# Performance work log

Hardware: AMD Instinct MI355X
Metric: run time of the kernel (lower is better)

The kernel has to match this reference:

```python
import jax, jax.numpy as jnp
import numpy as np

N_NODES = 50000
N_REL = 3
N_EDGES = 640000
D_IN = 128
D_HID = 128
D_OUT = 32
N_LAYERS = 2


def setup_inputs() -> dict:
    key = jax.random.key(0)
    ks = jax.random.split(key, 7)
    x = jax.random.normal(ks[0], (N_NODES, D_IN), dtype=jnp.float32)
    edge_index = jax.random.randint(ks[1], (N_REL, 2, N_EDGES), 0, N_NODES, dtype=jnp.int32)
    sc = 1.0 / np.sqrt(D_HID)
    W_neigh = jax.random.normal(ks[2], (N_LAYERS, N_REL, D_IN, D_HID), dtype=jnp.float32) * sc
    W_root = jax.random.normal(ks[3], (N_LAYERS, N_REL, D_IN, D_HID), dtype=jnp.float32) * sc
    b_conv = jax.random.normal(ks[4], (N_LAYERS, N_REL, D_HID), dtype=jnp.float32) * sc
    lin_W = jax.random.normal(ks[5], (D_HID, D_OUT), dtype=jnp.float32) * sc
    lin_b = jax.random.normal(ks[6], (D_OUT,), dtype=jnp.float32) * sc
    return {"x": x, "edge_index": edge_index, "W_neigh": W_neigh,
            "W_root": W_root, "b_conv": b_conv, "lin_W": lin_W, "lin_b": lin_b}


def _sage_hetero_layer(h, edge_index, Wn_l, Wr_l, b_l):
    # h: [N, d_in]; edge_index: [n_rel, 2, E]
    N = h.shape[0]
    acc = jnp.zeros((N, Wn_l.shape[-1]), dtype=h.dtype)
    for r in range(edge_index.shape[0]):  # small fixed relation set
        src, dst = edge_index[r, 0], edge_index[r, 1]
        msg = h[src]                                         # gather [E, d]
        summed = jax.ops.segment_sum(msg, dst, num_segments=N)
        deg = jax.ops.segment_sum(jnp.ones(src.shape, h.dtype), dst, num_segments=N)
        mean = summed / jnp.maximum(deg, 1.0)[:, None]       # SAGE mean aggr
        # SAGEConv: lin_l(aggr) + lin_r(x); bias lives in lin_l
        acc = acc + mean @ Wn_l[r] + h @ Wr_l[r] + b_l[r]    # HeteroConv sum across relations
    return acc


def reference(x, edge_index, W_neigh, W_root, b_conv, lin_W, lin_b):
    h = x
    for l in range(W_neigh.shape[0]):
        h = jax.nn.relu(_sage_hetero_layer(h, edge_index, W_neigh[l], W_root[l], b_conv[l]))
    return h @ lin_W + lin_b
```

## Files before the change

### kernel.cpp

```cpp
#include <hip/hip_runtime.h>

#define NN 50000
#define NE 640000
#define NR 3
#define DH 128
#define ET (NR * NE)

#define BK 256
#define NBK 196
#define NBT (NR * NBK)
#define NCH 512
#define CH (ET / NCH)
#define CAPB 4096

typedef __attribute__((ext_vector_type(8))) short short8;
typedef __attribute__((ext_vector_type(4))) float f32x4;
typedef __attribute__((ext_vector_type(2))) float f32x2;

__device__ __forceinline__ float bf2f(uint u) { return __uint_as_float(u << 16); }
__device__ __forceinline__ uint f2bf(float f) {
    uint u = __float_as_uint(f);
    u += 0x7fff + ((u >> 16) & 1);
    return u >> 16;
}
__device__ __forceinline__ uint pack2(float a, float b) { return f2bf(a) | (f2bf(b) << 16); }
__device__ __forceinline__ uint pk2t(float a, float b) {
    return __builtin_amdgcn_perm(__float_as_uint(b), __float_as_uint(a), 0x07060302u);
}
__device__ __forceinline__ f32x2 pkadd(f32x2 a, f32x2 b) {
    f32x2 d;
    asm("v_pk_add_f32 %0, %1, %2" : "=v"(d) : "v"(a), "v"(b));
    return d;
}
__device__ __forceinline__ f32x2 f8lo(uint u) {
    return __builtin_amdgcn_cvt_pk_f32_fp8(u, false);
}
__device__ __forceinline__ f32x2 f8hi(uint u) {
    return __builtin_amdgcn_cvt_pk_f32_fp8(u, true);
}
__device__ __forceinline__ uint pack4f8(float a, float b, float c, float d) {
    int w = __builtin_amdgcn_cvt_pk_fp8_f32(a, b, 0, false);
    w = __builtin_amdgcn_cvt_pk_fp8_f32(c, d, w, true);
    return (uint)w;
}

__global__ __launch_bounds__(256) void prep_hist(const float* __restrict__ x,
                                                 const int* __restrict__ ei,
                                                 const float* __restrict__ Wn,
                                                 const float* __restrict__ Wr,
                                                 const float* __restrict__ bc,
                                                 const float* __restrict__ linW,
                                                 unsigned char* __restrict__ xf8,
                                                 ushort* __restrict__ Wpack,
                                                 float* __restrict__ bsum,
                                                 int* __restrict__ gcnt) {
    int bid = blockIdx.x;
    int t = threadIdx.x;
    if (bid < NCH) {
        __shared__ int hist[NBT];
        for (int i = t; i < NBT; i += 256) hist[i] = 0;
        __syncthreads();
        int e0 = bid * CH;
        for (int i = t; i < CH; i += 256) {
            int e = e0 + i;
            int r = (e >= 2 * NE) ? 2 : (e >= NE ? 1 : 0);
            int le = e - r * NE;
            int dst = ei[r * 2 * NE + NE + le];
            atomicAdd(&hist[r * NBK + (dst >> 8)], 1);
        }
        __syncthreads();
        for (int i = t; i < NBT; i += 256) gcnt[bid * NBT + i] = hist[i];
    } else if (bid < NCH + 6251) {
        int gid = (bid - NCH) * 256 + t;
        if (gid >= NN * DH / 4) return;
        float4 v = ((const float4*)x)[gid];
        ((uint*)xf8)[gid] = pack4f8(v.x, v.y, v.z, v.w);
    } else if (bid < NCH + 6251 + 66) {
        int tid = (bid - NCH - 6251) * 256 + t;
        if (tid >= 264 * 64) return;
        int f = tid >> 6, lane = tid & 63;
        int l15 = lane & 15, l4 = lane >> 4;
        ushort hi8[8], lo8[8];
        if (f < 256) {
            int layer = f >> 7, seg = (f >> 5) & 3, kc = (f >> 3) & 3, nb = f & 7;
            int col = nb * 16 + l15;
            int kb = kc * 32 + l4 * 8;
#pragma unroll
            for (int e = 0; e < 8; ++e) {
                int k = kb + e;
                float v;
                if (seg < 3) {
                    v = Wn[(((size_t)layer * 3 + seg) * 128 + k) * 128 + col];
                } else {
                    const float* base = Wr + (size_t)layer * 3 * 16384;
                    v = base[k * 128 + col] + base[16384 + k * 128 + col] +
                        base[32768 + k * 128 + col];
                }
                uint h = f2bf(v);
                float rem = v - bf2f(h);
                hi8[e] = (ushort)h;
                lo8[e] = (ushort)f2bf(rem);
            }
        } else {
            int g = f - 256;
            int kc = g >> 1, nb = g & 1;
            int col = nb * 16 + l15;
            int kb = kc * 32 + l4 * 8;
#pragma unroll
            for (int e = 0; e < 8; ++e) {
                float v = linW[(kb + e) * 32 + col];
                uint h = f2bf(v);
                float rem = v - bf2f(h);
                hi8[e] = (ushort)h;
                lo8[e] = (ushort)f2bf(rem);
            }
        }
        *(short8*)(Wpack + (size_t)f * 1024 + lane * 8) = *(short8*)hi8;
        *(short8*)(Wpack + (size_t)f * 1024 + 512 + lane * 8) = *(short8*)lo8;
    } else {
        int l = t >> 7, j = t & 127;
        const float* bb = bc + l * 3 * DH;
        bsum[t] = bb[j] + bb[DH + j] + bb[2 * DH + j];
    }
}

__global__ __launch_bounds__(256) void cscan_kernel(const int* __restrict__ gcnt,
                                                    int* __restrict__ gbase,
                                                    int* __restrict__ btot) {
    int b = blockIdx.x, t = threadIdx.x;
    int v0 = gcnt[(2 * t) * NBT + b];
    int v1 = gcnt[(2 * t + 1) * NBT + b];
    int s = v0 + v1;
    int lane = t & 63, w = t >> 6;
    int sc = s;
#pragma unroll
    for (int d = 1; d < 64; d <<= 1) {
        int u = __shfl_up(sc, d);
        if (lane >= d) sc += u;
    }
    __shared__ int ws[4];
    if (lane == 63) ws[w] = sc;
    __syncthreads();
    int add = 0;
#pragma unroll
    for (int q = 0; q < 3; ++q)
        if (q < w) add += ws[q];
    int incl = sc + add;
    int excl = incl - s;
    gbase[(2 * t) * NBT + b] = excl;
    gbase[(2 * t + 1) * NBT + b] = excl + v0;
    if (t == 255) btot[b] = incl;
}

__global__ __launch_bounds__(256) void scatter_kernel(const int* __restrict__ ei,
                                                      const int* __restrict__ gbase,
                                                      uint* __restrict__ pairs) {
    __shared__ int cur[NBT];
    int g = blockIdx.x, t = threadIdx.x;
    for (int i = t; i < NBT; i += 256) cur[i] = i * CAPB + gbase[g * NBT + i];
    __syncthreads();
    int e0 = g * CH;
    for (int i = t; i < CH; i += 256) {
        int e = e0 + i;
        int r = (e >= 2 * NE) ? 2 : (e >= NE ? 1 : 0);
        int le = e - r * NE;
        int src = ei[r * 2 * NE + le];
        int dst = ei[r * 2 * NE + NE + le];
        int b = r * NBK + (dst >> 8);
        int pos = atomicAdd(&cur[b], 1);
        pairs[pos] = ((uint)src << 8) | (uint)(dst & 255u);
    }
}

__global__ __launch_bounds__(256) void csr_kernel(const uint* __restrict__ pairs,
                                                  const int* __restrict__ btot,
                                                  int* __restrict__ csr,
                                                  int2* __restrict__ od) {
    int b = blockIdx.x;
    int r = b / NBK;
    int n0 = (b - r * NBK) * BK;
    int cnt = btot[b];
    int base = b * CAPB;
    int t = threadIdx.x;

    __shared__ int hist[BK];
    __shared__ int cur[BK];
    __shared__ int ws[4];
    hist[t] = 0;
    __syncthreads();
    const uint* pp = pairs + base;
    for (int i = t; i < cnt; i += 256) atomicAdd(&hist[pp[i] & 255u], 1);
    __syncthreads();

    int lane = t & 63, w = t >> 6;
    int v = hist[t], s = v;
#pragma unroll
    for (int d = 1; d < 64; d <<= 1) {
        int u = __shfl_up(s, d);
        if (lane >= d) s += u;
    }
    if (lane == 63) ws[w] = s;
    __syncthreads();
    int add = 0;
#pragma unroll
    for (int q = 0; q < 3; ++q)
        if (q < w) add += ws[q];
    int excl = s + add - v;

    int node = n0 + t;
    if (node < NN) od[r * NN + node] = make_int2(base + excl, v);
    cur[t] = excl;
    __syncthreads();

    for (int i = t; i < cnt; i += 256) {
        uint pk = pp[i];
        int pos = atomicAdd(&cur[pk & 255u], 1);
        csr[base + pos] = (int)(pk >> 8);
    }
}

__global__ __launch_bounds__(256) void aggr_kernel(const unsigned char* __restrict__ tb8,
                                                   unsigned char* __restrict__ mean8,
                                                   const int* __restrict__ csr,
                                                   const int2* __restrict__ od) {
    int gtask = (blockIdx.x * 256 + threadIdx.x) >> 3;
    if (gtask >= NR * NN) return;
    int cs = threadIdx.x & 7;
    int2 v2 = od[gtask];
    int base = v2.x, d = v2.y;
    const int* lst = csr + base;
    const unsigned char* tbc = tb8 + cs * 16;

    f32x2 a2[8] = {{0.f, 0.f}, {0.f, 0.f}, {0.f, 0.f}, {0.f, 0.f},
                   {0.f, 0.f}, {0.f, 0.f}, {0.f, 0.f}, {0.f, 0.f}};
    for (int e = 0; e < d; e += 8) {
        uint4 q[8];
#pragma unroll
        for (int k = 0; k < 8; ++k) {
            int ee = e + k;
            int idx = lst[min(ee, d - 1)];
            uint4 v = *(const uint4*)(tbc + (size_t)idx * DH);
            bool ok = ee < d;
            q[k].x = ok ? v.x : 0u;
            q[k].y = ok ? v.y : 0u;
            q[k].z = ok ? v.z : 0u;
            q[k].w = ok ? v.w : 0u;
        }
#pragma unroll
        for (int k = 0; k < 8; ++k) {
            a2[0] = pkadd(a2[0], f8lo(q[k].x));
            a2[1] = pkadd(a2[1], f8hi(q[k].x));
            a2[2] = pkadd(a2[2], f8lo(q[k].y));
            a2[3] = pkadd(a2[3], f8hi(q[k].y));
            a2[4] = pkadd(a2[4], f8lo(q[k].z));
            a2[5] = pkadd(a2[5], f8hi(q[k].z));
            a2[6] = pkadd(a2[6], f8lo(q[k].w));
            a2[7] = pkadd(a2[7], f8hi(q[k].w));
        }
    }
    float inv = 1.f / fmaxf((float)d, 1.f);
    uint4 o;
    o.x = pack4f8(a2[0].x * inv, a2[0].y * inv, a2[1].x * inv, a2[1].y * inv);
    o.y = pack4f8(a2[2].x * inv, a2[2].y * inv, a2[3].x * inv, a2[3].y * inv);
    o.z = pack4f8(a2[4].x * inv, a2[4].y * inv, a2[5].x * inv, a2[5].y * inv);
    o.w = pack4f8(a2[6].x * inv, a2[6].y * inv, a2[7].x * inv, a2[7].y * inv);
    *(uint4*)(mean8 + (size_t)gtask * DH + cs * 16) = o;
}

template <bool LAST>
__global__ __launch_bounds__(256) void gemm_mfma(
    const float* __restrict__ xroot,
    const ushort* __restrict__ tbroot,
    const unsigned char* __restrict__ mean8,
    void* __restrict__ h_out,
    unsigned char* __restrict__ h1f8,
    const ushort* __restrict__ Wp,
    const float* __restrict__ bsum,
    const ushort* __restrict__ lWp,
    const float* __restrict__ linb)
{
    __shared__ ushort As[64][136];

    const int t = threadIdx.x, lane = t & 63, w = t >> 6;
    const int l15 = lane & 15, l4 = lane >> 4;
    const int row0 = blockIdx.x * 64;

    f32x4 acc[4][2];
    {
        float4 b0 = *(const float4*)(bsum + (2 * w) * 16 + l4 * 4);
        float4 b1 = *(const float4*)(bsum + (2 * w + 1) * 16 + l4 * 4);
#pragma unroll
        for (int rt = 0; rt < 4; ++rt) {
            acc[rt][0] = f32x4{b0.x, b0.y, b0.z, b0.w};
            acc[rt][1] = f32x4{b1.x, b1.y, b1.z, b1.w};
        }
    }

    for (int seg = 0; seg < 4; ++seg) {
        __syncthreads();
        if (seg < NR) {
#pragma unroll
            for (int i = 0; i < 2; ++i) {
                int q = i * 256 + t;
                int r = q >> 3, c = q & 7;
                int node = row0 + r;
                uint4 o0 = make_uint4(0, 0, 0, 0), o1 = make_uint4(0, 0, 0, 0);
                if (node < NN) {
                    uint4 v = *(const uint4*)(mean8 + ((size_t)seg * NN + node) * DH + c * 16);
                    f32x2 lo, hi;
                    lo = f8lo(v.x); hi = f8hi(v.x);
                    o0.x = pk2t(lo.x, lo.y); o0.y = pk2t(hi.x, hi.y);
                    lo = f8lo(v.y); hi = f8hi(v.y);
                    o0.z = pk2t(lo.x, lo.y); o0.w = pk2t(hi.x, hi.y);
                    lo = f8lo(v.z); hi = f8hi(v.z);
                    o1.x = pk2t(lo.x, lo.y); o1.y = pk2t(hi.x, hi.y);
                    lo = f8lo(v.w); hi = f8hi(v.w);
                    o1.z = pk2t(lo.x, lo.y); o1.w = pk2t(hi.x, hi.y);
                }
                *(uint4*)(&As[r][c * 16]) = o0;
                *(uint4*)(&As[r][c * 16 + 8]) = o1;
            }
        } else {
#pragma unroll
            for (int i = 0; i < 4; ++i) {
                int q = i * 256 + t;
                int r = q >> 4, c = q & 15;
                int node = row0 + r;
                uint4 v = make_uint4(0, 0, 0, 0);
                if (node < NN) {
                    if constexpr (!LAST) {
                        float4 f0 = *(const float4*)(xroot + (size_t)node * DH + c * 8);
                        float4 f1 = *(const float4*)(xroot + (size_t)node * DH + c * 8 + 4);
                        v.x = pack2(f0.x, f0.y);
                        v.y = pack2(f0.z, f0.w);
                        v.z = pack2(f1.x, f1.y);
                        v.w = pack2(f1.z, f1.w);
                    } else {
                        v = *(const uint4*)(tbroot + (size_t)node * DH + c * 8);
                    }
                }
                *(uint4*)(&As[r][c * 8]) = v;
            }
        }
        __syncthreads();
        const ushort* wseg = Wp + (size_t)seg * 32768;
#pragma unroll
        for (int kc = 0; kc < 4; ++kc) {
            const ushort* wkc = wseg + kc * 8192;
            short8 bh0 = *(const short8*)(wkc + (2 * w) * 1024 + lane * 8);
            short8 bl0 = *(const short8*)(wkc + (2 * w) * 1024 + 512 + lane * 8);
            short8 bh1 = *(const short8*)(wkc + (2 * w + 1) * 1024 + lane * 8);
            short8 bl1 = *(const short8*)(wkc + (2 * w + 1) * 1024 + 512 + lane * 8);
#pragma unroll
            for (int rt = 0; rt < 4; ++rt) {
                short8 a = *(const short8*)(&As[rt * 16 + l15][kc * 32 + l4 * 8]);
                acc[rt][0] = __builtin_amdgcn_mfma_f32_16x16x32_bf16(bh0, a, acc[rt][0], 0, 0, 0);
                acc[rt][0] = __builtin_amdgcn_mfma_f32_16x16x32_bf16(bl0, a, acc[rt][0], 0, 0, 0);
                acc[rt][1] = __builtin_amdgcn_mfma_f32_16x16x32_bf16(bh1, a, acc[rt][1], 0, 0, 0);
                acc[rt][1] = __builtin_amdgcn_mfma_f32_16x16x32_bf16(bl1, a, acc[rt][1], 0, 0, 0);
            }
        }
    }

    if constexpr (!LAST) {
        ushort* hb = (ushort*)h_out;
#pragma unroll
        for (int rt = 0; rt < 4; ++rt) {
            int node = row0 + rt * 16 + l15;
            if (node < NN) {
#pragma unroll
                for (int j = 0; j < 2; ++j) {
                    int c0 = (2 * w + j) * 16 + l4 * 4;
                    float r0 = fmaxf(acc[rt][j][0], 0.f);
                    float r1 = fmaxf(acc[rt][j][1], 0.f);
                    float r2 = fmaxf(acc[rt][j][2], 0.f);
                    float r3 = fmaxf(acc[rt][j][3], 0.f);
                    uint2 o;
                    o.x = pack2(r0, r1);
                    o.y = pack2(r2, r3);
                    *(uint2*)(hb + (size_t)node * DH + c0) = o;
                    *(uint*)(h1f8 + (size_t)node * DH + c0) = pack4f8(r0, r1, r2, r3);
                }
            }
        }
    } else {
        __syncthreads();
#pragma unroll
        for (int rt = 0; rt < 4; ++rt) {
            int rl = rt * 16 + l15;
#pragma unroll
            for (int j = 0; j < 2; ++j) {
                int c0 = (2 * w + j) * 16 + l4 * 4;
                uint2 o;
                o.x = pack2(fmaxf(acc[rt][j][0], 0.f), fmaxf(acc[rt][j][1], 0.f));
                o.y = pack2(fmaxf(acc[rt][j][2], 0.f), fmaxf(acc[rt][j][3], 0.f));
                *(uint2*)(&As[rl][c0]) = o;
            }
        }
        __syncthreads();
        f32x4 acc2[2];
        {
            float4 c0 = *(const float4*)(linb + l4 * 4);
            float4 c1 = *(const float4*)(linb + 16 + l4 * 4);
            acc2[0] = f32x4{c0.x, c0.y, c0.z, c0.w};
            acc2[1] = f32x4{c1.x, c1.y, c1.z, c1.w};
        }
#pragma unroll
        for (int kc = 0; kc < 4; ++kc) {
            short8 a = *(const short8*)(&As[w * 16 + l15][kc * 32 + l4 * 8]);
#pragma unroll
            for (int j = 0; j < 2; ++j) {
                short8 bh = *(const short8*)(lWp + (kc * 2 + j) * 1024 + lane * 8);
                short8 bl = *(const short8*)(lWp + (kc * 2 + j) * 1024 + 512 + lane * 8);
                acc2[j] = __builtin_amdgcn_mfma_f32_16x16x32_bf16(bh, a, acc2[j], 0, 0, 0);
                acc2[j] = __builtin_amdgcn_mfma_f32_16x16x32_bf16(bl, a, acc2[j], 0, 0, 0);
            }
        }
        float* outp = (float*)h_out;
        int node = row0 + w * 16 + l15;
        if (node < NN) {
#pragma unroll
            for (int j = 0; j < 2; ++j) {
                *(f32x4*)(outp + (size_t)node * 32 + j * 16 + l4 * 4) = acc2[j];
            }
        }
    }
}

extern "C" void kernel_launch(void* const* d_in, const int* in_sizes, int n_in,
                              void* d_out, int out_size, void* d_ws, size_t ws_size,
                              hipStream_t stream) {
    const float* x = (const float*)d_in[0];
    const int* ei = (const int*)d_in[1];
    const float* Wn = (const float*)d_in[2];
    const float* Wr = (const float*)d_in[3];
    const float* bc = (const float*)d_in[4];
    const float* linW = (const float*)d_in[5];
    const float* linb = (const float*)d_in[6];
    float* out = (float*)d_out;

    char* p = (char*)d_ws;
    int* gcnt = (int*)p;     p += (size_t)NCH * NBT * 4;
    int* gbase = (int*)p;    p += (size_t)NCH * NBT * 4;
    int* btot = (int*)p;     p += 4096;
    int2* od = (int2*)p;     p += (size_t)NR * NN * 8;
    int* csr = (int*)p;      p += (size_t)NBT * CAPB * 4;
    ushort* Wpack = (ushort*)p; p += (size_t)264 * 1024 * 2;
    float* bsum = (float*)p; p += 4096;
    unsigned char* f8tab = (unsigned char*)p; p += (size_t)NN * DH;
    ushort* h1b = (ushort*)p; p += (size_t)NN * DH * 2;
    unsigned char* mean8 = (unsigned char*)p; p += (size_t)NR * NN * DH;
    uint* pairs = (uint*)mean8;

    prep_hist<<<NCH + 6251 + 66 + 1, 256, 0, stream>>>(x, ei, Wn, Wr, bc, linW,
                                                       f8tab, Wpack, bsum, gcnt);
    cscan_kernel<<<NBT, 256, 0, stream>>>(gcnt, gbase, btot);
    scatter_kernel<<<NCH, 256, 0, stream>>>(ei, gbase, pairs);
    csr_kernel<<<NBT, 256, 0, stream>>>(pairs, btot, csr, od);

    int lb = (NN + 63) / 64;
    int ag = (NR * NN * 8 + 255) / 256;

    aggr_kernel<<<ag, 256, 0, stream>>>(f8tab, mean8, csr, od);
    gemm_mfma<false><<<lb, 256, 0, stream>>>(x, nullptr, mean8, h1b, f8tab,
                                             Wpack, bsum, nullptr, nullptr);
    aggr_kernel<<<ag, 256, 0, stream>>>(f8tab, mean8, csr, od);
    gemm_mfma<true><<<lb, 256, 0, stream>>>(nullptr, h1b, mean8, out, nullptr,
                                            Wpack + (size_t)128 * 1024, bsum + DH,
                                            Wpack + (size_t)256 * 1024, linb);
}
```

Measured before the change: 153.3 us.

## Fuse CSR-building kernels into one cooperative kernel with grid syncs

```diff
diff --git a/kernel.cpp b/kernel.cpp
--- a/kernel.cpp
+++ b/kernel.cpp
@@ -1,4 +1,7 @@
 #include <hip/hip_runtime.h>
+#include <hip/hip_cooperative_groups.h>
+
+namespace cg = cooperative_groups;
 
 #define NN 50000
 #define NE 640000
@@ -124,98 +127,94 @@
     }
 }
 
-__global__ __launch_bounds__(256) void cscan_kernel(const int* __restrict__ gcnt,
-                                                    int* __restrict__ gbase,
-                                                    int* __restrict__ btot) {
-    int b = blockIdx.x, t = threadIdx.x;
-    int v0 = gcnt[(2 * t) * NBT + b];
-    int v1 = gcnt[(2 * t + 1) * NBT + b];
-    int s = v0 + v1;
-    int lane = t & 63, w = t >> 6;
-    int sc = s;
-#pragma unroll
-    for (int d = 1; d < 64; d <<= 1) {
-        int u = __shfl_up(sc, d);
-        if (lane >= d) sc += u;
-    }
+__global__ __launch_bounds__(256) void build_csr(const int* __restrict__ ei,
+                                                 const int* __restrict__ gcnt,
+                                                 int* __restrict__ gbase,
+                                                 int* __restrict__ btot,
+                                                 uint* __restrict__ pairs,
+                                                 int* __restrict__ csr,
+                                                 int2* __restrict__ od) {
+    cg::grid_group grid = cg::this_grid();
+    const int b = blockIdx.x, t = threadIdx.x;
+    const int lane = t & 63, w = t >> 6;
+    __shared__ int sm[NBT];
+    __shared__ int sh[BK];
+    __shared__ int sc2[BK];
     __shared__ int ws[4];
-    if (lane == 63) ws[w] = sc;
-    __syncthreads();
-    int add = 0;
-#pragma unroll
-    for (int q = 0; q < 3; ++q)
-        if (q < w) add += ws[q];
-    int incl = sc + add;
-    int excl = incl - s;
-    gbase[(2 * t) * NBT + b] = excl;
-    gbase[(2 * t + 1) * NBT + b] = excl + v0;
-    if (t == 255) btot[b] = incl;
-}
-
-__global__ __launch_bounds__(256) void scatter_kernel(const int* __restrict__ ei,
-                                                      const int* __restrict__ gbase,
-                                                      uint* __restrict__ pairs) {
-    __shared__ int cur[NBT];
-    int g = blockIdx.x, t = threadIdx.x;
-    for (int i = t; i < NBT; i += 256) cur[i] = i * CAPB + gbase[g * NBT + i];
-    __syncthreads();
-    int e0 = g * CH;
-    for (int i = t; i < CH; i += 256) {
-        int e = e0 + i;
-        int r = (e >= 2 * NE) ? 2 : (e >= NE ? 1 : 0);
-        int le = e - r * NE;
-        int src = ei[r * 2 * NE + le];
-        int dst = ei[r * 2 * NE + NE + le];
-        int b = r * NBK + (dst >> 8);
-        int pos = atomicAdd(&cur[b], 1);
-        pairs[pos] = ((uint)src << 8) | (uint)(dst & 255u);
-    }
-}
-
-__global__ __launch_bounds__(256) void csr_kernel(const uint* __restrict__ pairs,
-                                                  const int* __restrict__ btot,
-                                                  int* __restrict__ csr,
-                                                  int2* __restrict__ od) {
-    int b = blockIdx.x;
-    int r = b / NBK;
-    int n0 = (b - r * NBK) * BK;
-    int cnt = btot[b];
-    int base = b * CAPB;
-    int t = threadIdx.x;
-
-    __shared__ int hist[BK];
-    __shared__ int cur[BK];
-    __shared__ int ws[4];
-    hist[t] = 0;
-    __syncthreads();
-    const uint* pp = pairs + base;
-    for (int i = t; i < cnt; i += 256) atomicAdd(&hist[pp[i] & 255u], 1);
-    __syncthreads();
-
-    int lane = t & 63, w = t >> 6;
-    int v = hist[t], s = v;
-#pragma unroll
-    for (int d = 1; d < 64; d <<= 1) {
-        int u = __shfl_up(s, d);
-        if (lane >= d) s += u;
-    }
-    if (lane == 63) ws[w] = s;
-    __syncthreads();
-    int add = 0;
-#pragma unroll
-    for (int q = 0; q < 3; ++q)
-        if (q < w) add += ws[q];
-    int excl = s + add - v;
-
-    int node = n0 + t;
-    if (node < NN) od[r * NN + node] = make_int2(base + excl, v);
-    cur[t] = excl;
-    __syncthreads();
-
-    for (int i = t; i < cnt; i += 256) {
-        uint pk = pp[i];
-        int pos = atomicAdd(&cur[pk & 255u], 1);
-        csr[base + pos] = (int)(pk >> 8);
+
+    {
+        int v0 = gcnt[(2 * t) * NBT + b];
+        int v1 = gcnt[(2 * t + 1) * NBT + b];
+        int s = v0 + v1;
+        int sc = s;
+#pragma unroll
+        for (int d = 1; d < 64; d <<= 1) {
+            int u = __shfl_up(sc, d);
+            if (lane >= d) sc += u;
+        }
+        if (lane == 63) ws[w] = sc;
+        __syncthreads();
+        int add = 0;
+#pragma unroll
+        for (int q = 0; q < 3; ++q)
+            if (q < w) add += ws[q];
+        int incl = sc + add;
+        int excl = incl - s;
+        gbase[(2 * t) * NBT + b] = excl;
+        gbase[(2 * t + 1) * NBT + b] = excl + v0;
+        if (t == 255) btot[b] = incl;
+    }
+    grid.sync();
+
+    if (b < NCH) {
+        for (int i = t; i < NBT; i += 256) sm[i] = i * CAPB + gbase[b * NBT + i];
+        __syncthreads();
+        int e0 = b * CH;
+        for (int i = t; i < CH; i += 256) {
+            int e = e0 + i;
+            int r = (e >= 2 * NE) ? 2 : (e >= NE ? 1 : 0);
+            int le = e - r * NE;
+            int src = ei[r * 2 * NE + le];
+            int dst = ei[r * 2 * NE + NE + le];
+            int bk = r * NBK + (dst >> 8);
+            int pos = atomicAdd(&sm[bk], 1);
+            pairs[pos] = ((uint)src << 8) | (uint)(dst & 255u);
+        }
+    }
+    grid.sync();
+
+    {
+        int r = b / NBK;
+        int n0 = (b - r * NBK) * BK;
+        int cnt = btot[b];
+        int base = b * CAPB;
+        sh[t] = 0;
+        __syncthreads();
+        const uint* pp = pairs + base;
+        for (int i = t; i < cnt; i += 256) atomicAdd(&sh[pp[i] & 255u], 1);
+        __syncthreads();
+        int v = sh[t], s = v;
+#pragma unroll
+        for (int d = 1; d < 64; d <<= 1) {
+            int u = __shfl_up(s, d);
+            if (lane >= d) s += u;
+        }
+        if (lane == 63) ws[w] = s;
+        __syncthreads();
+        int add = 0;
+#pragma unroll
+        for (int q = 0; q < 3; ++q)
+            if (q < w) add += ws[q];
+        int excl = s + add - v;
+        int node = n0 + t;
+        if (node < NN) od[r * NN + node] = make_int2(base + excl, v);
+        sc2[t] = excl;
+        __syncthreads();
+        for (int i = t; i < cnt; i += 256) {
+            uint pk = pp[i];
+            int pos = atomicAdd(&sc2[pk & 255u], 1);
+            csr[base + pos] = (int)(pk >> 8);
+        }
     }
 }
 
@@ -454,9 +453,11 @@
 
     prep_hist<<<NCH + 6251 + 66 + 1, 256, 0, stream>>>(x, ei, Wn, Wr, bc, linW,
                                                        f8tab, Wpack, bsum, gcnt);
-    cscan_kernel<<<NBT, 256, 0, stream>>>(gcnt, gbase, btot);
-    scatter_kernel<<<NCH, 256, 0, stream>>>(ei, gbase, pairs);
-    csr_kernel<<<NBT, 256, 0, stream>>>(pairs, btot, csr, od);
+    {
+        void* args[] = {(void*)&ei,   (void*)&gcnt, (void*)&gbase, (void*)&btot,
+                        (void*)&pairs,(void*)&csr,  (void*)&od};
+        hipLaunchCooperativeKernel((void*)build_csr, dim3(NBT), dim3(256), args, 0, stream);
+    }
 
     int lb = (NN + 63) / 64;
     int ag = (NR * NN * 8 + 255) / 256;
```

Result: slower. 300.1 us (+95.8%).
